# Kernel tuning notes

Measured on AMD Instinct MI355X. Metric: run time of the kernel, lower is better.

## Reference

```python
import jax, jax.numpy as jnp
import numpy as np

B, C, S = 16, 8, 128
DT, DX, DY = 0.001, 1.0, 1.0
NUM_STEPS = 10
EPS = 1e-6


def _thomas(a, b, c, d):
    """Batched Thomas tridiagonal solve. a,b,c,d: [M,N] rows; solve along N."""
    aT, bT, cT, dT = a.T, b.T, c.T, d.T  # [N, M]
    zero = jnp.zeros_like(dT[0])

    def fwd(carry, inp):
        cs_p, ds_p = carry
        ai, bi, ci, di = inp
        denom = bi - ai * cs_p + EPS  # i=0: cs_p=0 -> denom = b0 + eps (matches torch)
        cs = ci / denom
        ds = (di - ai * ds_p) / denom
        return (cs, ds), (cs, ds)

    _, (c_star, d_star) = jax.lax.scan(fwd, (zero, zero), (aT, bT, cT, dT))

    def bwd(x_next, inp):
        ci, di = inp
        x = di - ci * x_next
        return x, x

    _, xs = jax.lax.scan(bwd, d_star[-1], (c_star[:-1], d_star[:-1]), reverse=True)
    x = jnp.concatenate([xs, d_star[-1:]], axis=0)  # [N, M]
    return x.T


def _diffuse_rows(u2d, coeff):
    """Implicit 1D diffusion along last axis. u2d, coeff: [M,N]."""
    a = -coeff
    c = -coeff
    b = 1.0 + 2.0 * coeff
    b = b.at[:, 0].set(1.0 + coeff[:, 0])
    b = b.at[:, -1].set(1.0 + coeff[:, -1])
    return _thomas(a, b, c, u2d)


def _forward(u, alpha_base, beta_base, alpha_time_coeff, beta_time_coeff, channel_mixing):
    Bb, Cc, H, W = u.shape
    half = DT / 2.0
    t = 0.0
    for _ in range(NUM_STEPS):
        # x half-step (coefficient alpha at time t)
        alpha = jnp.clip(alpha_base + alpha_time_coeff * t, EPS, 10.0)
        u = jnp.einsum('dc,bchw->bdhw', channel_mixing, u)
        uf = u.reshape(Bb * Cc, H, W)
        af = jnp.broadcast_to(alpha[None], (Bb, Cc, H, W)).reshape(Bb * Cc, H, W)
        uf = _diffuse_rows(uf.reshape(-1, W), af.reshape(-1, W) * half / DX**2).reshape(Bb * Cc, H, W)
        t += half
        # y full step (coefficient beta at time t+dt/2)
        beta = jnp.clip(beta_base + beta_time_coeff * t, EPS, 10.0)
        bf = jnp.broadcast_to(beta[None], (Bb, Cc, H, W)).reshape(Bb * Cc, H, W)
        ut = uf.transpose(0, 2, 1).reshape(-1, H)
        bt = bf.transpose(0, 2, 1).reshape(-1, H)
        ut = _diffuse_rows(ut, bt * DT / DY**2)
        uf = ut.reshape(Bb * Cc, W, H).transpose(0, 2, 1)
        t += half
        # x half-step (coefficient alpha at time t+dt)
        alpha = jnp.clip(alpha_base + alpha_time_coeff * t, EPS, 10.0)
        af = jnp.broadcast_to(alpha[None], (Bb, Cc, H, W)).reshape(Bb * Cc, H, W)
        uf = _diffuse_rows(uf.reshape(-1, W), af.reshape(-1, W) * half / DX**2).reshape(Bb * Cc, H, W)
        u = uf.reshape(Bb, Cc, H, W)
    return u


def setup_inputs() -> dict:
    key = jax.random.key(0)
    k_u, k_cm, k_atc, k_btc = jax.random.split(key, 4)
    u = jax.random.normal(k_u, (B, C, S, S), dtype=jnp.float32)
    alpha_base = jnp.ones((C, S, S), dtype=jnp.float32)
    beta_base = jnp.ones((C, S, S), dtype=jnp.float32)
    alpha_time_coeff = jax.random.normal(k_atc, (C, S, S), dtype=jnp.float32) * 0.01
    beta_time_coeff = jax.random.normal(k_btc, (C, S, S), dtype=jnp.float32) * 0.01
    channel_mixing = jnp.eye(C, dtype=jnp.float32) + jax.random.normal(k_cm, (C, C), dtype=jnp.float32) * 0.01
    return {
        'u': u,
        'alpha_base': alpha_base,
        'beta_base': beta_base,
        'alpha_time_coeff': alpha_time_coeff,
        'beta_time_coeff': beta_time_coeff,
        'channel_mixing': channel_mixing,
    }


def reference(u, alpha_base, beta_base, alpha_time_coeff, beta_time_coeff, channel_mixing):
    return _forward(u, alpha_base, beta_base, alpha_time_coeff, beta_time_coeff, channel_mixing)
```

## Files before the change

### kernel.cpp

```cpp
#include <hip/hip_runtime.h>
#include <hip/hip_fp16.h>


constexpr int S_  = 128;
constexpr int RS  = 129;
constexpr float EPSF = 1e-6f;
constexpr int CSS = 8 * 128 * 128;

constexpr int SOFF_A = 0;
constexpr int SOFF_B = 64 * 128;
constexpr int SOFF_C = 128 * 128;
constexpr int SPOOL  = 192 * 128;

__device__ __forceinline__ int swad(int r, int b) {
    return r * 128 + (((b) ^ (r & 31)) << 2);
}

template <int N>
__device__ __forceinline__ void jrunN(const float (&e)[N], const float (&g)[N],
                                      float (&o)[N - 4]) {
    float x1[N];
    #pragma unroll
    for (int i = 1; i <= N - 2; ++i) x1[i] = fmaf(g[i], e[i - 1] + e[i + 1], e[i]);
    #pragma unroll
    for (int i = 2; i <= N - 3; ++i) o[i - 2] = fmaf(g[i], x1[i - 1] + x1[i + 1], e[i]);
}

__global__ __launch_bounds__(256) void coef_kernel(
    const float* __restrict__ ab, const float* __restrict__ atc,
    const float* __restrict__ bb, const float* __restrict__ btc,
    __half2* __restrict__ cf)
{
    for (int gc = blockIdx.x * 256 + threadIdx.x; gc < CSS; gc += gridDim.x * 256) {
        const int w = gc & 127, h = (gc >> 7) & 127;
        const float abv = ab[gc], atv = atc[gc], bbv = bb[gc], btv = btc[gc];
        const float nbY = (h == 0 || h == S_ - 1) ? 1.f : 2.f;
        const float nbX = (w == 0 || w == S_ - 1) ? 1.f : 2.f;
        for (int k = 0; k < 10; ++k) {
            const float ty = (2 * k + 1) * 0.0005f;
            const float tx = (2 * k + 2) * 0.0005f;
            float be = fminf(fmaxf(fmaf(btv, ty, bbv), EPSF), 10.f);
            float co = be * 0.001f;
            float rb = __builtin_amdgcn_rcpf(fmaf(nbY, co, 1.f) + EPSF);
            cf[k * CSS + gc] = __floats2half2_rn(rb * co, rb - 1.f);
            float al = fminf(fmaxf(fmaf(atv, tx, abv), EPSF), 10.f);
            co = al * 0.0005f;
            rb = __builtin_amdgcn_rcpf(fmaf(nbX, co, 1.f) + EPSF);
            cf[(10 + k) * CSS + gc] = __floats2half2_rn(rb * co, rb - 1.f);
        }
        float al = fminf(fmaxf(abv, EPSF), 10.f);
        float co = al * 0.0005f;
        float rb = __builtin_amdgcn_rcpf(fmaf(nbX, co, 1.f) + EPSF);
        cf[20 * CSS + gc] = __floats2half2_rn(rb * co, rb - 1.f);
    }
}

__global__ __launch_bounds__(512, 2) void head_kernel(
    const float* __restrict__ u0, __half* __restrict__ ud,
    const __half2* __restrict__ cfy, const __half2* __restrict__ cfx,
    const __half2* __restrict__ cfx0, const float* __restrict__ cm)
{
    constexpr int POOL   = 288 * RS;
    constexpr int OFF_A  = 0;
    constexpr int OFF_B  = 64 * RS;
    constexpr int OFF_CP = 192 * RS;
    constexpr int OFF_X0 = 96 * RS;
    __shared__ float sP[POOL];
    const int tid = threadIdx.x;
    const int b   = blockIdx.x >> 4;
    const int h0  = (blockIdx.x & 15) << 3;

    #pragma unroll
    for (int m = 0; m < 2; ++m) {
        const int col = tid + 512 * m;
        const int c = col >> 7, w = col & 127;
        #pragma unroll
        for (int hh = 0; hh < 12; ++hh) {
            const int gh = h0 - 2 + hh;
            float v = 0.f;
            if (gh >= 0 && gh < S_) v = u0[((b * 8 + c) * S_ + gh) * S_ + w];
            sP[(c * 12 + hh) * RS + w] = v;
        }
    }
    #pragma unroll
    for (int m = 0; m < 12; ++m) {
        const int task = tid + 512 * m;
        const int r = task >> 6, col2 = task & 63;
        const int c = r / 12, hh = r % 12;
        int gh = h0 - 2 + hh; gh = gh < 0 ? 0 : (gh >= S_ ? S_ - 1 : gh);
        const uint2 v = ((const uint2*)cfx0)[(c * S_ + gh) * 64 + col2];
        sP[OFF_CP + r * RS + col2 * 2]     = __uint_as_float(v.x);
        sP[OFF_CP + r * RS + col2 * 2 + 1] = __uint_as_float(v.y);
    }
    __syncthreads();
    {
        float M[64];
        #pragma unroll
        for (int i = 0; i < 64; ++i) M[i] = cm[i];
        #pragma unroll
        for (int m = 0; m < 3; ++m) {
            const int p = tid + 512 * m;
            const int hh = p >> 7, w = p & 127;
            float v[8], o[8];
            #pragma unroll
            for (int c = 0; c < 8; ++c) v[c] = sP[(c * 12 + hh) * RS + w];
            #pragma unroll
            for (int dd = 0; dd < 8; ++dd) {
                float a = 0.f;
                #pragma unroll
                for (int c = 0; c < 8; ++c) a = fmaf(M[dd * 8 + c], v[c], a);
                o[dd] = a;
            }
            #pragma unroll
            for (int c = 0; c < 8; ++c) sP[(c * 12 + hh) * RS + w] = o[c];
        }
    }
    __syncthreads();
    #pragma unroll
    for (int m = 0; m < 3; ++m) {
        const int task = tid + 512 * m;
        const int r96 = task % 96, wr = task / 96;
        const int hh = r96 % 12;
        const int gh = h0 - 2 + hh;
        const bool rowin = (gh >= 0 && gh < S_);
        const int w0 = wr * 8;
        float e[12], g[12];
        #pragma unroll
        for (int j = 0; j < 12; ++j) {
            const int wj = w0 - 2 + j;
            const bool win = (wj >= 0 && wj < S_);
            const float dv = win ? sP[r96 * RS + wj] : 0.f;
            uint cb = (rowin && win) ? __float_as_uint(sP[OFF_CP + r96 * RS + wj]) : 0u;
            const float2 f = __half22float2(*reinterpret_cast<__half2*>(&cb));
            e[j] = (1.f + f.y) * dv;
            g[j] = f.x;
        }
        float o[8]; jrunN<12>(e, g, o);
        #pragma unroll
        for (int i = 0; i < 8; ++i) sP[OFF_X0 + r96 * RS + w0 + i] = o[i];
    }
    __syncthreads();

    #pragma unroll
    for (int m = 0; m < 2; ++m) {
        const int col = tid + 512 * m;
        const int c = col >> 7, w = col & 127;
        float e[12], g[12];
        #pragma unroll
        for (int hh = 0; hh < 12; ++hh) {
            const int gh = h0 - 2 + hh;
            const bool inr = (gh >= 0 && gh < S_);
            const int ghc = inr ? gh : 0;
            const float dv = sP[OFF_X0 + (c * 12 + hh) * RS + w];
            const float2 f = __half22float2(cfy[(c * S_ + ghc) * S_ + w]);
            e[hh] = (1.f + f.y) * dv;
            g[hh] = inr ? f.x : 0.f;
        }
        float o[8]; jrunN<12>(e, g, o);
        #pragma unroll
        for (int i = 0; i < 8; ++i) sP[OFF_A + (c * 8 + i) * RS + w] = o[i];
    }
    __syncthreads();
    #pragma unroll
    for (int m = 0; m < 8; ++m) {
        const int task = tid + 512 * m;
        const int r = task >> 6, col2 = task & 63;
        const int c = r >> 3, ho = r & 7;
        const uint2 v = ((const uint2*)cfx)[(c * S_ + h0 + ho) * 64 + col2];
        sP[OFF_CP + r * RS + col2 * 2]     = __uint_as_float(v.x);
        sP[OFF_CP + r * RS + col2 * 2 + 1] = __uint_as_float(v.y);
    }
    __syncthreads();

    float rbk[2][12], gk[2][12], xo[2][8];
    #pragma unroll
    for (int m = 0; m < 2; ++m) {
        const int run = tid + 512 * m;
        const int r = run & 63, wr = run >> 6;
        const int w0 = wr * 8;
        float e[12];
        #pragma unroll
        for (int j = 0; j < 12; ++j) {
            const int wj = w0 - 2 + j;
            const bool win = (wj >= 0 && wj < S_);
            const float dv = win ? sP[OFF_A + r * RS + wj] : 0.f;
            uint cb = win ? __float_as_uint(sP[OFF_CP + r * RS + wj]) : 0u;
            const float2 f = __half22float2(*reinterpret_cast<__half2*>(&cb));
            rbk[m][j] = 1.f + f.y; gk[m][j] = f.x;
            e[j] = rbk[m][j] * dv;
        }
        jrunN<12>(e, gk[m], xo[m]);
    }
    #pragma unroll
    for (int m = 0; m < 2; ++m) {
        const int run = tid + 512 * m;
        const int r = run & 63, w0 = (run >> 6) * 8;
        #pragma unroll
        for (int i = 0; i < 8; ++i) sP[OFF_B + r * RS + w0 + i] = xo[m][i];
    }
    __syncthreads();
    {
        float M[64];
        #pragma unroll
        for (int i = 0; i < 64; ++i) M[i] = cm[i];
        #pragma unroll
        for (int m = 0; m < 2; ++m) {
            const int p = tid + 512 * m;
            const int ho = p >> 7, w = p & 127;
            float v[8], o[8];
            #pragma unroll
            for (int c = 0; c < 8; ++c) v[c] = sP[OFF_B + (c * 8 + ho) * RS + w];
            #pragma unroll
            for (int dd = 0; dd < 8; ++dd) {
                float a = 0.f;
                #pragma unroll
                for (int c = 0; c < 8; ++c) a = fmaf(M[dd * 8 + c], v[c], a);
                o[dd] = a;
            }
            #pragma unroll
            for (int c = 0; c < 8; ++c) sP[OFF_A + (c * 8 + ho) * RS + w] = o[c];
        }
    }
    __syncthreads();
    #pragma unroll
    for (int m = 0; m < 2; ++m) {
        const int run = tid + 512 * m;
        const int r = run & 63, wr = run >> 6;
        const int w0 = wr * 8;
        const int c = r >> 3, ho = r & 7;
        float e[12];
        #pragma unroll
        for (int j = 0; j < 12; ++j) {
            const int wj = w0 - 2 + j;
            const bool win = (wj >= 0 && wj < S_);
            const float dv = win ? sP[OFF_A + r * RS + wj] : 0.f;
            e[j] = rbk[m][j] * dv;
        }
        float o[8]; jrunN<12>(e, gk[m], o);
        __half2* d2 = (__half2*)&ud[((b * 8 + c) * S_ + h0 + ho) * S_ + w0];
        d2[0] = __floats2half2_rn(o[0], o[1]);
        d2[1] = __floats2half2_rn(o[2], o[3]);
        d2[2] = __floats2half2_rn(o[4], o[5]);
        d2[3] = __floats2half2_rn(o[6], o[7]);
    }
}

template <bool LASTK>
__global__ __launch_bounds__(512) void stepS_kernel(
    const __half* __restrict__ us, void* __restrict__ udst_,
    const __half2* __restrict__ cfy, const __half2* __restrict__ cfx,
    const float* __restrict__ cm)
{
    __shared__ __align__(16) float sP[SPOOL];
    const int tid = threadIdx.x;
    const int b   = blockIdx.x >> 4;
    const int h0  = (blockIdx.x & 15) << 3;

    {
        const int c  = tid >> 6;
        const int wp = tid & 63;
        const int wbase = 2 * wp;
        uint du[12]; uint2 dc[12];
        #pragma unroll
        for (int hh = 0; hh < 12; ++hh) {
            const int gh = h0 - 2 + hh;
            const bool inr = (gh >= 0 && gh < S_);
            const int ghc = inr ? gh : 0;
            du[hh] = inr ? *(const uint*)&us[((b * 8 + c) * S_ + ghc) * S_ + wbase] : 0u;
            dc[hh] = *(const uint2*)&cfy[(c * S_ + ghc) * S_ + wbase];
        }
        float o2[2][8];
        #pragma unroll
        for (int s = 0; s < 2; ++s) {
            float e[12], g[12];
            #pragma unroll
            for (int hh = 0; hh < 12; ++hh) {
                const int gh = h0 - 2 + hh;
                const bool inr = (gh >= 0 && gh < S_);
                uint ub = du[hh];
                __half2 hu = *reinterpret_cast<__half2*>(&ub);
                const float dv = s ? __high2float(hu) : __low2float(hu);
                uint cb = s ? dc[hh].y : dc[hh].x;
                const float2 f = __half22float2(*reinterpret_cast<__half2*>(&cb));
                e[hh] = (1.f + f.y) * dv;
                g[hh] = inr ? f.x : 0.f;
            }
            jrunN<12>(e, g, o2[s]);
        }
        #pragma unroll
        for (int i = 0; i < 8; ++i) {
            const int r = c * 8 + i;
            float2* p = (float2*)&sP[SOFF_A + r * 128 +
                                     (((wp >> 1) ^ (r & 31)) << 2) + 2 * (wp & 1)];
            *p = make_float2(o2[0][i], o2[1][i]);
        }
    }
    {
        const uint* cfxu = (const uint*)cfx;
        #pragma unroll
        for (int m = 0; m < 4; ++m) {
            const int task = tid + 512 * m;
            const int r = task >> 5, col4 = task & 31;
            const int c = r >> 3, ho = r & 7;
            const uint4 v = *(const uint4*)&cfxu[(c * S_ + h0 + ho) * S_ + col4 * 4];
            *(float4*)&sP[SOFF_C + swad(r, col4)] =
                make_float4(__uint_as_float(v.x), __uint_as_float(v.y),
                            __uint_as_float(v.z), __uint_as_float(v.w));
        }
    }
    __syncthreads();

    float rbk[2][12], gk[2][12], xo[2][8];
    #pragma unroll
    for (int m = 0; m < 2; ++m) {
        const int r  = tid & 63;
        const int wr = (tid >> 6) + 8 * m;
        const int w0 = wr * 8;
        float f[16]; uint cb[16];
        #pragma unroll
        for (int i = 0; i < 4; ++i) {
            const int bb = (w0 >> 2) - 1 + i;
            if (bb >= 0 && bb < 32) {
                const float4 va = *(const float4*)&sP[SOFF_A + swad(r, bb)];
                const float4 vc = *(const float4*)&sP[SOFF_C + swad(r, bb)];
                f[4 * i + 0] = va.x; f[4 * i + 1] = va.y;
                f[4 * i + 2] = va.z; f[4 * i + 3] = va.w;
                cb[4 * i + 0] = __float_as_uint(vc.x);
                cb[4 * i + 1] = __float_as_uint(vc.y);
                cb[4 * i + 2] = __float_as_uint(vc.z);
                cb[4 * i + 3] = __float_as_uint(vc.w);
            } else {
                f[4 * i + 0] = f[4 * i + 1] = f[4 * i + 2] = f[4 * i + 3] = 0.f;
                cb[4 * i + 0] = cb[4 * i + 1] = cb[4 * i + 2] = cb[4 * i + 3] = 0u;
            }
        }
        float e[12];
        #pragma unroll
        for (int j = 0; j < 12; ++j) {
            uint c_ = cb[j + 2];
            const float2 fc = __half22float2(*reinterpret_cast<__half2*>(&c_));
            rbk[m][j] = 1.f + fc.y; gk[m][j] = fc.x;
            e[j] = rbk[m][j] * f[j + 2];
        }
        jrunN<12>(e, gk[m], xo[m]);
    }

    if (LASTK) {
        float* ud = (float*)udst_;
        #pragma unroll
        for (int m = 0; m < 2; ++m) {
            const int r  = tid & 63;
            const int wr = (tid >> 6) + 8 * m;
            const int c = r >> 3, ho = r & 7;
            float4* dst4 = (float4*)&ud[((b * 8 + c) * S_ + h0 + ho) * S_ + wr * 8];
            dst4[0] = make_float4(xo[m][0], xo[m][1], xo[m][2], xo[m][3]);
            dst4[1] = make_float4(xo[m][4], xo[m][5], xo[m][6], xo[m][7]);
        }
    } else {
        #pragma unroll
        for (int m = 0; m < 2; ++m) {
            const int r  = tid & 63;
            const int wr = (tid >> 6) + 8 * m;
            *(float4*)&sP[SOFF_B + swad(r, 2 * wr)] =
                make_float4(xo[m][0], xo[m][1], xo[m][2], xo[m][3]);
            *(float4*)&sP[SOFF_B + swad(r, 2 * wr + 1)] =
                make_float4(xo[m][4], xo[m][5], xo[m][6], xo[m][7]);
        }
        __syncthreads();
        {
            float M[64];
            #pragma unroll
            for (int i = 0; i < 64; ++i) M[i] = cm[i];
            #pragma unroll
            for (int m = 0; m < 2; ++m) {
                const int p = tid + 512 * m;
                const int ho = p >> 7, w = p & 127;
                float v[8], o[8];
                #pragma unroll
                for (int c = 0; c < 8; ++c) {
                    const int r = c * 8 + ho;
                    v[c] = sP[SOFF_B + r * 128 + (((w >> 2) ^ (r & 31)) << 2) + (w & 3)];
                }
                #pragma unroll
                for (int dd = 0; dd < 8; ++dd) {
                    float a = 0.f;
                    #pragma unroll
                    for (int c = 0; c < 8; ++c) a = fmaf(M[dd * 8 + c], v[c], a);
                    o[dd] = a;
                }
                #pragma unroll
                for (int c = 0; c < 8; ++c) {
                    const int r = c * 8 + ho;
                    sP[SOFF_A + r * 128 + (((w >> 2) ^ (r & 31)) << 2) + (w & 3)] = o[c];
                }
            }
        }
        __syncthreads();
        __half* ud = (__half*)udst_;
        #pragma unroll
        for (int m = 0; m < 2; ++m) {
            const int r  = tid & 63;
            const int wr = (tid >> 6) + 8 * m;
            const int w0 = wr * 8;
            const int c = r >> 3, ho = r & 7;
            float f[16];
            #pragma unroll
            for (int i = 0; i < 4; ++i) {
                const int bb = (w0 >> 2) - 1 + i;
                if (bb >= 0 && bb < 32) {
                    const float4 va = *(const float4*)&sP[SOFF_A + swad(r, bb)];
                    f[4 * i + 0] = va.x; f[4 * i + 1] = va.y;
                    f[4 * i + 2] = va.z; f[4 * i + 3] = va.w;
                } else {
                    f[4 * i + 0] = f[4 * i + 1] = f[4 * i + 2] = f[4 * i + 3] = 0.f;
                }
            }
            float e[12];
            #pragma unroll
            for (int j = 0; j < 12; ++j) e[j] = rbk[m][j] * f[j + 2];
            float o[8]; jrunN<12>(e, gk[m], o);
            __half2 q0 = __floats2half2_rn(o[0], o[1]);
            __half2 q1 = __floats2half2_rn(o[2], o[3]);
            __half2 q2 = __floats2half2_rn(o[4], o[5]);
            __half2 q3 = __floats2half2_rn(o[6], o[7]);
            uint4 pk;
            pk.x = *reinterpret_cast<uint*>(&q0);
            pk.y = *reinterpret_cast<uint*>(&q1);
            pk.z = *reinterpret_cast<uint*>(&q2);
            pk.w = *reinterpret_cast<uint*>(&q3);
            *(uint4*)&ud[((b * 8 + c) * S_ + h0 + ho) * S_ + w0] = pk;
        }
    }
}

extern "C" void kernel_launch(void* const* d_in, const int* in_sizes, int n_in,
                              void* d_out, int out_size, void* d_ws, size_t ws_size,
                              hipStream_t stream) {
    const float* u_in = (const float*)d_in[0];
    const float* ab   = (const float*)d_in[1];
    const float* bbta = (const float*)d_in[2];
    const float* atc  = (const float*)d_in[3];
    const float* btc  = (const float*)d_in[4];
    const float* cm   = (const float*)d_in[5];
    float* uo = (float*)d_out;
    __half*  h1 = (__half*)d_ws;
    __half*  h2 = (__half*)((char*)d_ws + (8u << 20));
    __half2* cf = (__half2*)((char*)d_ws + (16u << 20));

    coef_kernel<<<dim3(512), dim3(256), 0, stream>>>(ab, atc, bbta, btc, cf);

    const dim3 g(256), blk(512);
    head_kernel<<<g, blk, 0, stream>>>(u_in, h1, cf + 0 * CSS, cf + 10 * CSS,
                                       cf + 20 * CSS, cm);
    const __half* s = h1; __half* d = h2;
    for (int k = 1; k <= 8; ++k) {
        stepS_kernel<false><<<g, blk, 0, stream>>>(s, d, cf + k * CSS,
                                                   cf + (10 + k) * CSS, cm);
        const __half* ns = d;
        d = (d == h2) ? h1 : h2;
        s = ns;
    }
    stepS_kernel<true><<<g, blk, 0, stream>>>(s, uo, cf + 9 * CSS,
                                              cf + 19 * CSS, cm);
}
```

Baseline: 152.7 us.

## Fuse time steps in pairs per kernel and fold coefficient computation into head

Replaces the per-step kernel chain with a kernel that advances two ADI steps per launch, using a wider halo (16 rows) in the y direction so the two steps can run without touching global memory in between. The separate coefficient kernel is removed: the head kernel computes the coefficients for its own first steps inline and writes the tables for later steps. This cuts the launch count from 11 to 5 and halves the fp16 intermediate traffic to global memory, at the cost of redundant halo computation, more shared memory (288 rows) and more register pressure.

```diff
diff --git a/kernel.cpp b/kernel.cpp
--- a/kernel.cpp
+++ b/kernel.cpp
@@ -3,17 +3,20 @@
 
 
 constexpr int S_  = 128;
-constexpr int RS  = 129;
 constexpr float EPSF = 1e-6f;
 constexpr int CSS = 8 * 128 * 128;
 
-constexpr int SOFF_A = 0;
-constexpr int SOFF_B = 64 * 128;
-constexpr int SOFF_C = 128 * 128;
-constexpr int SPOOL  = 192 * 128;
-
-__device__ __forceinline__ int swad(int r, int b) {
-    return r * 128 + (((b) ^ (r & 31)) << 2);
+constexpr int P0    = 0;
+constexpr int Q0    = 96 * 128;
+constexpr int C0    = 192 * 128;
+constexpr int ST0   = 96 * 128;
+constexpr int SPOOL = 288 * 128;
+
+__device__ __forceinline__ int swad4(int r, int b4) {
+    return r * 128 + (((b4) ^ (r & 31)) << 2);
+}
+__device__ __forceinline__ int swadw(int r, int w) {
+    return r * 128 + ((((w) >> 2) ^ (r & 31)) << 2) + ((w) & 3);
 }
 
 template <int N>
@@ -26,229 +29,29 @@
     for (int i = 2; i <= N - 3; ++i) o[i - 2] = fmaf(g[i], x1[i - 1] + x1[i + 1], e[i]);
 }
 
-__global__ __launch_bounds__(256) void coef_kernel(
-    const float* __restrict__ ab, const float* __restrict__ atc,
-    const float* __restrict__ bb, const float* __restrict__ btc,
-    __half2* __restrict__ cf)
-{
-    for (int gc = blockIdx.x * 256 + threadIdx.x; gc < CSS; gc += gridDim.x * 256) {
-        const int w = gc & 127, h = (gc >> 7) & 127;
-        const float abv = ab[gc], atv = atc[gc], bbv = bb[gc], btv = btc[gc];
-        const float nbY = (h == 0 || h == S_ - 1) ? 1.f : 2.f;
-        const float nbX = (w == 0 || w == S_ - 1) ? 1.f : 2.f;
-        for (int k = 0; k < 10; ++k) {
-            const float ty = (2 * k + 1) * 0.0005f;
-            const float tx = (2 * k + 2) * 0.0005f;
-            float be = fminf(fmaxf(fmaf(btv, ty, bbv), EPSF), 10.f);
-            float co = be * 0.001f;
-            float rb = __builtin_amdgcn_rcpf(fmaf(nbY, co, 1.f) + EPSF);
-            cf[k * CSS + gc] = __floats2half2_rn(rb * co, rb - 1.f);
-            float al = fminf(fmaxf(fmaf(atv, tx, abv), EPSF), 10.f);
-            co = al * 0.0005f;
-            rb = __builtin_amdgcn_rcpf(fmaf(nbX, co, 1.f) + EPSF);
-            cf[(10 + k) * CSS + gc] = __floats2half2_rn(rb * co, rb - 1.f);
-        }
-        float al = fminf(fmaxf(abv, EPSF), 10.f);
-        float co = al * 0.0005f;
-        float rb = __builtin_amdgcn_rcpf(fmaf(nbX, co, 1.f) + EPSF);
-        cf[20 * CSS + gc] = __floats2half2_rn(rb * co, rb - 1.f);
-    }
-}
-
-__global__ __launch_bounds__(512, 2) void head_kernel(
-    const float* __restrict__ u0, __half* __restrict__ ud,
-    const __half2* __restrict__ cfy, const __half2* __restrict__ cfx,
-    const __half2* __restrict__ cfx0, const float* __restrict__ cm)
-{
-    constexpr int POOL   = 288 * RS;
-    constexpr int OFF_A  = 0;
-    constexpr int OFF_B  = 64 * RS;
-    constexpr int OFF_CP = 192 * RS;
-    constexpr int OFF_X0 = 96 * RS;
-    __shared__ float sP[POOL];
-    const int tid = threadIdx.x;
-    const int b   = blockIdx.x >> 4;
-    const int h0  = (blockIdx.x & 15) << 3;
-
-    #pragma unroll
-    for (int m = 0; m < 2; ++m) {
-        const int col = tid + 512 * m;
-        const int c = col >> 7, w = col & 127;
-        #pragma unroll
-        for (int hh = 0; hh < 12; ++hh) {
-            const int gh = h0 - 2 + hh;
-            float v = 0.f;
-            if (gh >= 0 && gh < S_) v = u0[((b * 8 + c) * S_ + gh) * S_ + w];
-            sP[(c * 12 + hh) * RS + w] = v;
-        }
-    }
-    #pragma unroll
-    for (int m = 0; m < 12; ++m) {
-        const int task = tid + 512 * m;
-        const int r = task >> 6, col2 = task & 63;
-        const int c = r / 12, hh = r % 12;
-        int gh = h0 - 2 + hh; gh = gh < 0 ? 0 : (gh >= S_ ? S_ - 1 : gh);
-        const uint2 v = ((const uint2*)cfx0)[(c * S_ + gh) * 64 + col2];
-        sP[OFF_CP + r * RS + col2 * 2]     = __uint_as_float(v.x);
-        sP[OFF_CP + r * RS + col2 * 2 + 1] = __uint_as_float(v.y);
-    }
-    __syncthreads();
-    {
-        float M[64];
-        #pragma unroll
-        for (int i = 0; i < 64; ++i) M[i] = cm[i];
-        #pragma unroll
-        for (int m = 0; m < 3; ++m) {
-            const int p = tid + 512 * m;
-            const int hh = p >> 7, w = p & 127;
-            float v[8], o[8];
-            #pragma unroll
-            for (int c = 0; c < 8; ++c) v[c] = sP[(c * 12 + hh) * RS + w];
-            #pragma unroll
-            for (int dd = 0; dd < 8; ++dd) {
-                float a = 0.f;
-                #pragma unroll
-                for (int c = 0; c < 8; ++c) a = fmaf(M[dd * 8 + c], v[c], a);
-                o[dd] = a;
-            }
-            #pragma unroll
-            for (int c = 0; c < 8; ++c) sP[(c * 12 + hh) * RS + w] = o[c];
-        }
-    }
-    __syncthreads();
-    #pragma unroll
-    for (int m = 0; m < 3; ++m) {
-        const int task = tid + 512 * m;
-        const int r96 = task % 96, wr = task / 96;
-        const int hh = r96 % 12;
-        const int gh = h0 - 2 + hh;
-        const bool rowin = (gh >= 0 && gh < S_);
-        const int w0 = wr * 8;
-        float e[12], g[12];
-        #pragma unroll
-        for (int j = 0; j < 12; ++j) {
-            const int wj = w0 - 2 + j;
-            const bool win = (wj >= 0 && wj < S_);
-            const float dv = win ? sP[r96 * RS + wj] : 0.f;
-            uint cb = (rowin && win) ? __float_as_uint(sP[OFF_CP + r96 * RS + wj]) : 0u;
-            const float2 f = __half22float2(*reinterpret_cast<__half2*>(&cb));
-            e[j] = (1.f + f.y) * dv;
-            g[j] = f.x;
-        }
-        float o[8]; jrunN<12>(e, g, o);
-        #pragma unroll
-        for (int i = 0; i < 8; ++i) sP[OFF_X0 + r96 * RS + w0 + i] = o[i];
-    }
-    __syncthreads();
-
-    #pragma unroll
-    for (int m = 0; m < 2; ++m) {
-        const int col = tid + 512 * m;
-        const int c = col >> 7, w = col & 127;
-        float e[12], g[12];
-        #pragma unroll
-        for (int hh = 0; hh < 12; ++hh) {
-            const int gh = h0 - 2 + hh;
-            const bool inr = (gh >= 0 && gh < S_);
-            const int ghc = inr ? gh : 0;
-            const float dv = sP[OFF_X0 + (c * 12 + hh) * RS + w];
-            const float2 f = __half22float2(cfy[(c * S_ + ghc) * S_ + w]);
-            e[hh] = (1.f + f.y) * dv;
-            g[hh] = inr ? f.x : 0.f;
-        }
-        float o[8]; jrunN<12>(e, g, o);
-        #pragma unroll
-        for (int i = 0; i < 8; ++i) sP[OFF_A + (c * 8 + i) * RS + w] = o[i];
-    }
-    __syncthreads();
-    #pragma unroll
-    for (int m = 0; m < 8; ++m) {
-        const int task = tid + 512 * m;
-        const int r = task >> 6, col2 = task & 63;
-        const int c = r >> 3, ho = r & 7;
-        const uint2 v = ((const uint2*)cfx)[(c * S_ + h0 + ho) * 64 + col2];
-        sP[OFF_CP + r * RS + col2 * 2]     = __uint_as_float(v.x);
-        sP[OFF_CP + r * RS + col2 * 2 + 1] = __uint_as_float(v.y);
-    }
-    __syncthreads();
-
-    float rbk[2][12], gk[2][12], xo[2][8];
-    #pragma unroll
-    for (int m = 0; m < 2; ++m) {
-        const int run = tid + 512 * m;
-        const int r = run & 63, wr = run >> 6;
-        const int w0 = wr * 8;
-        float e[12];
-        #pragma unroll
-        for (int j = 0; j < 12; ++j) {
-            const int wj = w0 - 2 + j;
-            const bool win = (wj >= 0 && wj < S_);
-            const float dv = win ? sP[OFF_A + r * RS + wj] : 0.f;
-            uint cb = win ? __float_as_uint(sP[OFF_CP + r * RS + wj]) : 0u;
-            const float2 f = __half22float2(*reinterpret_cast<__half2*>(&cb));
-            rbk[m][j] = 1.f + f.y; gk[m][j] = f.x;
-            e[j] = rbk[m][j] * dv;
-        }
-        jrunN<12>(e, gk[m], xo[m]);
-    }
-    #pragma unroll
-    for (int m = 0; m < 2; ++m) {
-        const int run = tid + 512 * m;
-        const int r = run & 63, w0 = (run >> 6) * 8;
-        #pragma unroll
-        for (int i = 0; i < 8; ++i) sP[OFF_B + r * RS + w0 + i] = xo[m][i];
-    }
-    __syncthreads();
-    {
-        float M[64];
-        #pragma unroll
-        for (int i = 0; i < 64; ++i) M[i] = cm[i];
-        #pragma unroll
-        for (int m = 0; m < 2; ++m) {
-            const int p = tid + 512 * m;
-            const int ho = p >> 7, w = p & 127;
-            float v[8], o[8];
-            #pragma unroll
-            for (int c = 0; c < 8; ++c) v[c] = sP[OFF_B + (c * 8 + ho) * RS + w];
-            #pragma unroll
-            for (int dd = 0; dd < 8; ++dd) {
-                float a = 0.f;
-                #pragma unroll
-                for (int c = 0; c < 8; ++c) a = fmaf(M[dd * 8 + c], v[c], a);
-                o[dd] = a;
-            }
-            #pragma unroll
-            for (int c = 0; c < 8; ++c) sP[OFF_A + (c * 8 + ho) * RS + w] = o[c];
-        }
-    }
-    __syncthreads();
-    #pragma unroll
-    for (int m = 0; m < 2; ++m) {
-        const int run = tid + 512 * m;
-        const int r = run & 63, wr = run >> 6;
-        const int w0 = wr * 8;
-        const int c = r >> 3, ho = r & 7;
-        float e[12];
-        #pragma unroll
-        for (int j = 0; j < 12; ++j) {
-            const int wj = w0 - 2 + j;
-            const bool win = (wj >= 0 && wj < S_);
-            const float dv = win ? sP[OFF_A + r * RS + wj] : 0.f;
-            e[j] = rbk[m][j] * dv;
-        }
-        float o[8]; jrunN<12>(e, gk[m], o);
-        __half2* d2 = (__half2*)&ud[((b * 8 + c) * S_ + h0 + ho) * S_ + w0];
-        d2[0] = __floats2half2_rn(o[0], o[1]);
-        d2[1] = __floats2half2_rn(o[2], o[3]);
-        d2[2] = __floats2half2_rn(o[4], o[5]);
-        d2[3] = __floats2half2_rn(o[6], o[7]);
-    }
-}
-
-template <bool LASTK>
-__global__ __launch_bounds__(512) void stepS_kernel(
+#define TAPS_GATHER(REG_A, f, cb)                                              \
+    {                                                                          \
+        _Pragma("unroll")                                                      \
+        for (int i_ = 0; i_ < 4; ++i_) {                                       \
+            const int bb_ = 2 * wr - 1 + i_;                                   \
+            if (bb_ >= 0 && bb_ < 32) {                                        \
+                const float4 va_ = *(const float4*)&sP[(REG_A) + swad4(r, bb_)];\
+                const float4 vc_ = *(const float4*)&sP[C0 + swad4(r, bb_)];    \
+                f[4*i_+0]=va_.x; f[4*i_+1]=va_.y; f[4*i_+2]=va_.z; f[4*i_+3]=va_.w; \
+                cb[4*i_+0]=__float_as_uint(vc_.x); cb[4*i_+1]=__float_as_uint(vc_.y); \
+                cb[4*i_+2]=__float_as_uint(vc_.z); cb[4*i_+3]=__float_as_uint(vc_.w); \
+            } else {                                                           \
+                f[4*i_+0]=f[4*i_+1]=f[4*i_+2]=f[4*i_+3]=0.f;                   \
+                cb[4*i_+0]=cb[4*i_+1]=cb[4*i_+2]=cb[4*i_+3]=0u;                \
+            }                                                                  \
+        }                                                                      \
+    }
+
+template <bool LAST>
+__global__ __launch_bounds__(512) void pairS_kernel(
     const __half* __restrict__ us, void* __restrict__ udst_,
-    const __half2* __restrict__ cfy, const __half2* __restrict__ cfx,
+    const __half2* __restrict__ cfyA, const __half2* __restrict__ cfxA,
+    const __half2* __restrict__ cfyB, const __half2* __restrict__ cfxB,
     const float* __restrict__ cm)
 {
     __shared__ __align__(16) float sP[SPOOL];
@@ -257,25 +60,23 @@
     const int h0  = (blockIdx.x & 15) << 3;
 
     {
-        const int c  = tid >> 6;
-        const int wp = tid & 63;
-        const int wbase = 2 * wp;
-        uint du[12]; uint2 dc[12];
-        #pragma unroll
-        for (int hh = 0; hh < 12; ++hh) {
-            const int gh = h0 - 2 + hh;
+        const int c = tid >> 6, wp = tid & 63, wb = 2 * wp;
+        uint du[16]; uint2 dc[16];
+        #pragma unroll
+        for (int hh = 0; hh < 16; ++hh) {
+            const int gh = h0 - 4 + hh;
             const bool inr = (gh >= 0 && gh < S_);
             const int ghc = inr ? gh : 0;
-            du[hh] = inr ? *(const uint*)&us[((b * 8 + c) * S_ + ghc) * S_ + wbase] : 0u;
-            dc[hh] = *(const uint2*)&cfy[(c * S_ + ghc) * S_ + wbase];
-        }
-        float o2[2][8];
+            du[hh] = inr ? *(const uint*)&us[((b * 8 + c) * S_ + ghc) * S_ + wb] : 0u;
+            dc[hh] = *(const uint2*)&cfyA[(c * S_ + ghc) * S_ + wb];
+        }
+        float o2[2][12];
         #pragma unroll
         for (int s = 0; s < 2; ++s) {
-            float e[12], g[12];
-            #pragma unroll
-            for (int hh = 0; hh < 12; ++hh) {
-                const int gh = h0 - 2 + hh;
+            float e[16], g[16];
+            #pragma unroll
+            for (int hh = 0; hh < 16; ++hh) {
+                const int gh = h0 - 4 + hh;
                 const bool inr = (gh >= 0 && gh < S_);
                 uint ub = du[hh];
                 __half2 hu = *reinterpret_cast<__half2*>(&ub);
@@ -285,27 +86,140 @@
                 e[hh] = (1.f + f.y) * dv;
                 g[hh] = inr ? f.x : 0.f;
             }
+            jrunN<16>(e, g, o2[s]);
+        }
+        #pragma unroll
+        for (int i = 0; i < 12; ++i) {
+            const int r = c * 12 + i;
+            *(float2*)&sP[P0 + r * 128 + (((wp >> 1) ^ (r & 31)) << 2) + 2 * (wp & 1)]
+                = make_float2(o2[0][i], o2[1][i]);
+        }
+    }
+    {
+        const uint* cx = (const uint*)cfxA;
+        #pragma unroll
+        for (int m = 0; m < 6; ++m) {
+            const int task = tid + 512 * m;
+            const int r = task >> 5, b4 = task & 31;
+            const int c = r / 12, ha = r - c * 12;
+            int gh = h0 - 2 + ha; gh = gh < 0 ? 0 : (gh >= S_ ? S_ - 1 : gh);
+            const uint4 v = *(const uint4*)&cx[(c * S_ + gh) * S_ + b4 * 4];
+            *(float4*)&sP[C0 + swad4(r, b4)] = make_float4(
+                __uint_as_float(v.x), __uint_as_float(v.y),
+                __uint_as_float(v.z), __uint_as_float(v.w));
+        }
+    }
+    __syncthreads();
+
+    #pragma unroll
+    for (int m = 0; m < 3; ++m) {
+        const int r  = (tid & 31) + 32 * m;
+        const int wr = tid >> 5;
+        float f[16]; uint cb[16];
+        TAPS_GATHER(P0, f, cb)
+        float e[12], g[12];
+        #pragma unroll
+        for (int j = 0; j < 12; ++j) {
+            uint c_ = cb[j + 2];
+            const float2 fc = __half22float2(*reinterpret_cast<__half2*>(&c_));
+            e[j] = (1.f + fc.y) * f[j + 2];
+            g[j] = fc.x;
+        }
+        float o[8]; jrunN<12>(e, g, o);
+        *(float4*)&sP[Q0 + swad4(r, 2 * wr)]     = make_float4(o[0], o[1], o[2], o[3]);
+        *(float4*)&sP[Q0 + swad4(r, 2 * wr + 1)] = make_float4(o[4], o[5], o[6], o[7]);
+    }
+    __syncthreads();
+    {
+        float M[64];
+        #pragma unroll
+        for (int i = 0; i < 64; ++i) M[i] = cm[i];
+        #pragma unroll
+        for (int m = 0; m < 3; ++m) {
+            const int p = tid + 512 * m;
+            const int ha = p >> 7, w = p & 127;
+            float v[8], o[8];
+            #pragma unroll
+            for (int c = 0; c < 8; ++c) v[c] = sP[Q0 + swadw(c * 12 + ha, w)];
+            #pragma unroll
+            for (int dd = 0; dd < 8; ++dd) {
+                float a = 0.f;
+                #pragma unroll
+                for (int c = 0; c < 8; ++c) a = fmaf(M[dd * 8 + c], v[c], a);
+                o[dd] = a;
+            }
+            #pragma unroll
+            for (int c = 0; c < 8; ++c) sP[Q0 + swadw(c * 12 + ha, w)] = o[c];
+        }
+    }
+    __syncthreads();
+    #pragma unroll
+    for (int m = 0; m < 3; ++m) {
+        const int r  = (tid & 31) + 32 * m;
+        const int wr = tid >> 5;
+        float f[16]; uint cb[16];
+        TAPS_GATHER(Q0, f, cb)
+        float e[12], g[12];
+        #pragma unroll
+        for (int j = 0; j < 12; ++j) {
+            uint c_ = cb[j + 2];
+            const float2 fc = __half22float2(*reinterpret_cast<__half2*>(&c_));
+            e[j] = (1.f + fc.y) * f[j + 2];
+            g[j] = fc.x;
+        }
+        float o[8]; jrunN<12>(e, g, o);
+        *(float4*)&sP[P0 + swad4(r, 2 * wr)]     = make_float4(o[0], o[1], o[2], o[3]);
+        *(float4*)&sP[P0 + swad4(r, 2 * wr + 1)] = make_float4(o[4], o[5], o[6], o[7]);
+    }
+    __syncthreads();
+
+    {
+        const int c = tid >> 6, wp = tid & 63, wb = 2 * wp;
+        float2 dp[12]; uint2 dc[12];
+        #pragma unroll
+        for (int hh = 0; hh < 12; ++hh) {
+            const int gh = h0 - 2 + hh;
+            const bool inr = (gh >= 0 && gh < S_);
+            const int ghc = inr ? gh : 0;
+            const int r = c * 12 + hh;
+            dp[hh] = *(const float2*)&sP[P0 + r * 128 +
+                                         (((wp >> 1) ^ (r & 31)) << 2) + 2 * (wp & 1)];
+            dc[hh] = *(const uint2*)&cfyB[(c * S_ + ghc) * S_ + wb];
+        }
+        float o2[2][8];
+        #pragma unroll
+        for (int s = 0; s < 2; ++s) {
+            float e[12], g[12];
+            #pragma unroll
+            for (int hh = 0; hh < 12; ++hh) {
+                const int gh = h0 - 2 + hh;
+                const bool inr = (gh >= 0 && gh < S_);
+                const float dv = s ? dp[hh].y : dp[hh].x;
+                uint cb = s ? dc[hh].y : dc[hh].x;
+                const float2 f = __half22float2(*reinterpret_cast<__half2*>(&cb));
+                e[hh] = (1.f + f.y) * dv;
+                g[hh] = inr ? f.x : 0.f;
+            }
             jrunN<12>(e, g, o2[s]);
         }
         #pragma unroll
         for (int i = 0; i < 8; ++i) {
             const int r = c * 8 + i;
-            float2* p = (float2*)&sP[SOFF_A + r * 128 +
-                                     (((wp >> 1) ^ (r & 31)) << 2) + 2 * (wp & 1)];
-            *p = make_float2(o2[0][i], o2[1][i]);
-        }
-    }
-    {
-        const uint* cfxu = (const uint*)cfx;
+            *(float2*)&sP[Q0 + r * 128 + (((wp >> 1) ^ (r & 31)) << 2) + 2 * (wp & 1)]
+                = make_float2(o2[0][i], o2[1][i]);
+        }
+    }
+    {
+        const uint* cx = (const uint*)cfxB;
         #pragma unroll
         for (int m = 0; m < 4; ++m) {
             const int task = tid + 512 * m;
-            const int r = task >> 5, col4 = task & 31;
+            const int r = task >> 5, b4 = task & 31;
             const int c = r >> 3, ho = r & 7;
-            const uint4 v = *(const uint4*)&cfxu[(c * S_ + h0 + ho) * S_ + col4 * 4];
-            *(float4*)&sP[SOFF_C + swad(r, col4)] =
-                make_float4(__uint_as_float(v.x), __uint_as_float(v.y),
-                            __uint_as_float(v.z), __uint_as_float(v.w));
+            const uint4 v = *(const uint4*)&cx[(c * S_ + h0 + ho) * S_ + b4 * 4];
+            *(float4*)&sP[C0 + swad4(r, b4)] = make_float4(
+                __uint_as_float(v.x), __uint_as_float(v.y),
+                __uint_as_float(v.z), __uint_as_float(v.w));
         }
     }
     __syncthreads();
@@ -315,25 +229,8 @@
     for (int m = 0; m < 2; ++m) {
         const int r  = tid & 63;
         const int wr = (tid >> 6) + 8 * m;
-        const int w0 = wr * 8;
         float f[16]; uint cb[16];
-        #pragma unroll
-        for (int i = 0; i < 4; ++i) {
-            const int bb = (w0 >> 2) - 1 + i;
-            if (bb >= 0 && bb < 32) {
-                const float4 va = *(const float4*)&sP[SOFF_A + swad(r, bb)];
-                const float4 vc = *(const float4*)&sP[SOFF_C + swad(r, bb)];
-                f[4 * i + 0] = va.x; f[4 * i + 1] = va.y;
-                f[4 * i + 2] = va.z; f[4 * i + 3] = va.w;
-                cb[4 * i + 0] = __float_as_uint(vc.x);
-                cb[4 * i + 1] = __float_as_uint(vc.y);
-                cb[4 * i + 2] = __float_as_uint(vc.z);
-                cb[4 * i + 3] = __float_as_uint(vc.w);
-            } else {
-                f[4 * i + 0] = f[4 * i + 1] = f[4 * i + 2] = f[4 * i + 3] = 0.f;
-                cb[4 * i + 0] = cb[4 * i + 1] = cb[4 * i + 2] = cb[4 * i + 3] = 0u;
-            }
-        }
+        TAPS_GATHER(Q0, f, cb)
         float e[12];
         #pragma unroll
         for (int j = 0; j < 12; ++j) {
@@ -345,7 +242,7 @@
         jrunN<12>(e, gk[m], xo[m]);
     }
 
-    if (LASTK) {
+    if (LAST) {
         float* ud = (float*)udst_;
         #pragma unroll
         for (int m = 0; m < 2; ++m) {
@@ -361,10 +258,8 @@
         for (int m = 0; m < 2; ++m) {
             const int r  = tid & 63;
             const int wr = (tid >> 6) + 8 * m;
-            *(float4*)&sP[SOFF_B + swad(r, 2 * wr)] =
-                make_float4(xo[m][0], xo[m][1], xo[m][2], xo[m][3]);
-            *(float4*)&sP[SOFF_B + swad(r, 2 * wr + 1)] =
-                make_float4(xo[m][4], xo[m][5], xo[m][6], xo[m][7]);
+            *(float4*)&sP[P0 + swad4(r, 2 * wr)]     = make_float4(xo[m][0], xo[m][1], xo[m][2], xo[m][3]);
+            *(float4*)&sP[P0 + swad4(r, 2 * wr + 1)] = make_float4(xo[m][4], xo[m][5], xo[m][6], xo[m][7]);
         }
         __syncthreads();
         {
@@ -377,10 +272,7 @@
                 const int ho = p >> 7, w = p & 127;
                 float v[8], o[8];
                 #pragma unroll
-                for (int c = 0; c < 8; ++c) {
-                    const int r = c * 8 + ho;
-                    v[c] = sP[SOFF_B + r * 128 + (((w >> 2) ^ (r & 31)) << 2) + (w & 3)];
-                }
+                for (int c = 0; c < 8; ++c) v[c] = sP[P0 + swadw(c * 8 + ho, w)];
                 #pragma unroll
                 for (int dd = 0; dd < 8; ++dd) {
                     float a = 0.f;
@@ -389,10 +281,7 @@
                     o[dd] = a;
                 }
                 #pragma unroll
-                for (int c = 0; c < 8; ++c) {
-                    const int r = c * 8 + ho;
-                    sP[SOFF_A + r * 128 + (((w >> 2) ^ (r & 31)) << 2) + (w & 3)] = o[c];
-                }
+                for (int c = 0; c < 8; ++c) sP[P0 + swadw(c * 8 + ho, w)] = o[c];
             }
         }
         __syncthreads();
@@ -401,18 +290,16 @@
         for (int m = 0; m < 2; ++m) {
             const int r  = tid & 63;
             const int wr = (tid >> 6) + 8 * m;
-            const int w0 = wr * 8;
             const int c = r >> 3, ho = r & 7;
             float f[16];
             #pragma unroll
             for (int i = 0; i < 4; ++i) {
-                const int bb = (w0 >> 2) - 1 + i;
+                const int bb = 2 * wr - 1 + i;
                 if (bb >= 0 && bb < 32) {
-                    const float4 va = *(const float4*)&sP[SOFF_A + swad(r, bb)];
-                    f[4 * i + 0] = va.x; f[4 * i + 1] = va.y;
-                    f[4 * i + 2] = va.z; f[4 * i + 3] = va.w;
+                    const float4 va = *(const float4*)&sP[P0 + swad4(r, bb)];
+                    f[4*i+0]=va.x; f[4*i+1]=va.y; f[4*i+2]=va.z; f[4*i+3]=va.w;
                 } else {
-                    f[4 * i + 0] = f[4 * i + 1] = f[4 * i + 2] = f[4 * i + 3] = 0.f;
+                    f[4*i+0]=f[4*i+1]=f[4*i+2]=f[4*i+3]=0.f;
                 }
             }
             float e[12];
@@ -428,7 +315,380 @@
             pk.y = *reinterpret_cast<uint*>(&q1);
             pk.z = *reinterpret_cast<uint*>(&q2);
             pk.w = *reinterpret_cast<uint*>(&q3);
-            *(uint4*)&ud[((b * 8 + c) * S_ + h0 + ho) * S_ + w0] = pk;
+            *(uint4*)&ud[((b * 8 + c) * S_ + h0 + ho) * S_ + wr * 8] = pk;
+        }
+    }
+}
+
+__global__ __launch_bounds__(512) void head2_kernel(
+    const float* __restrict__ u0, __half* __restrict__ ud,
+    const float* __restrict__ ab, const float* __restrict__ atc,
+    const float* __restrict__ bb, const float* __restrict__ btc,
+    const float* __restrict__ cm, __half2* __restrict__ cf)
+{
+    __shared__ __align__(16) float sP[SPOOL];
+    const int tid = threadIdx.x;
+    const int b   = blockIdx.x >> 4;
+    const int h0  = (blockIdx.x & 15) << 3;
+    const float dt2 = 0.0005f;
+
+    #pragma unroll
+    for (int m = 0; m < 8; ++m) {
+        const int task = tid + 512 * m;
+        const int r = task >> 5, b4 = task & 31;
+        const int c = r >> 4, hh = r & 15;
+        const int gh = h0 - 4 + hh;
+        float4 v = make_float4(0.f, 0.f, 0.f, 0.f);
+        if (gh >= 0 && gh < S_) v = *(const float4*)&u0[((b * 8 + c) * S_ + gh) * S_ + 4 * b4];
+        *(float4*)&sP[ST0 + swad4(r, b4)] = v;
+    }
+    __syncthreads();
+    {
+        float M[64];
+        #pragma unroll
+        for (int i = 0; i < 64; ++i) M[i] = cm[i];
+        #pragma unroll
+        for (int m = 0; m < 4; ++m) {
+            const int p = tid + 512 * m;
+            const int hh = p >> 7, w = p & 127;
+            float v[8], o[8];
+            #pragma unroll
+            for (int c = 0; c < 8; ++c) v[c] = sP[ST0 + swadw(c * 16 + hh, w)];
+            #pragma unroll
+            for (int dd = 0; dd < 8; ++dd) {
+                float a = 0.f;
+                #pragma unroll
+                for (int c = 0; c < 8; ++c) a = fmaf(M[dd * 8 + c], v[c], a);
+                o[dd] = a;
+            }
+            #pragma unroll
+            for (int c = 0; c < 8; ++c) sP[ST0 + swadw(c * 16 + hh, w)] = o[c];
+        }
+    }
+    __syncthreads();
+    {
+        float xh[4][8];
+        #pragma unroll
+        for (int m = 0; m < 4; ++m) {
+            const int r  = (tid & 31) + 32 * m;
+            const int wr = tid >> 5;
+            const int w0 = wr * 8;
+            const int c = r >> 4, hh = r & 15;
+            const int gh = h0 - 4 + hh;
+            const bool rowin = (gh >= 0 && gh < S_);
+            float f[16];
+            #pragma unroll
+            for (int i = 0; i < 4; ++i) {
+                const int bb4 = 2 * wr - 1 + i;
+                if (bb4 >= 0 && bb4 < 32) {
+                    const float4 va = *(const float4*)&sP[ST0 + swad4(r, bb4)];
+                    f[4*i+0]=va.x; f[4*i+1]=va.y; f[4*i+2]=va.z; f[4*i+3]=va.w;
+                } else {
+                    f[4*i+0]=f[4*i+1]=f[4*i+2]=f[4*i+3]=0.f;
+                }
+            }
+            float e[12], g[12];
+            #pragma unroll
+            for (int j = 0; j < 12; ++j) {
+                const int wj = w0 - 2 + j;
+                const bool win = (wj >= 0 && wj < S_);
+                float co = 0.f;
+                if (rowin && win) {
+                    float al = ab[(c * S_ + gh) * S_ + wj];
+                    co = fminf(fmaxf(al, EPSF), 10.f) * 0.0005f;
+                }
+                const float nb = (wj == 0 || wj == S_ - 1) ? 1.f : 2.f;
+                const float rb = __builtin_amdgcn_rcpf(fmaf(nb, co, 1.f) + EPSF);
+                e[j] = rb * f[j + 2]; g[j] = rb * co;
+            }
+            jrunN<12>(e, g, xh[m]);
+        }
+        __syncthreads();
+        #pragma unroll
+        for (int m = 0; m < 4; ++m) {
+            const int r  = (tid & 31) + 32 * m;
+            const int wr = tid >> 5;
+            *(float4*)&sP[ST0 + swad4(r, 2 * wr)]     = make_float4(xh[m][0], xh[m][1], xh[m][2], xh[m][3]);
+            *(float4*)&sP[ST0 + swad4(r, 2 * wr + 1)] = make_float4(xh[m][4], xh[m][5], xh[m][6], xh[m][7]);
+        }
+    }
+    __syncthreads();
+    {
+        const int c = tid >> 6, wp = tid & 63, wb = 2 * wp;
+        float o2[2][12];
+        #pragma unroll
+        for (int s = 0; s < 2; ++s) {
+            float e[16], g[16];
+            #pragma unroll
+            for (int hh = 0; hh < 16; ++hh) {
+                const int gh = h0 - 4 + hh;
+                const bool inr = (gh >= 0 && gh < S_);
+                const int ghc = inr ? gh : 0;
+                const int r = c * 16 + hh;
+                const float2 d2 = *(const float2*)&sP[ST0 + r * 128 +
+                                    (((wp >> 1) ^ (r & 31)) << 2) + 2 * (wp & 1)];
+                const float dv = s ? d2.y : d2.x;
+                const float2 b2 = *(const float2*)&bb[(c * S_ + ghc) * S_ + wb];
+                const float2 t2 = *(const float2*)&btc[(c * S_ + ghc) * S_ + wb];
+                float be = fmaf(s ? t2.y : t2.x, 1 * dt2, s ? b2.y : b2.x);
+                be = fminf(fmaxf(be, EPSF), 10.f);
+                const float co = inr ? be * 0.001f : 0.f;
+                const float nb = (gh == 0 || gh == S_ - 1) ? 1.f : 2.f;
+                const float rb = __builtin_amdgcn_rcpf(fmaf(nb, co, 1.f) + EPSF);
+                e[hh] = rb * dv; g[hh] = rb * co;
+            }
+            jrunN<16>(e, g, o2[s]);
+        }
+        #pragma unroll
+        for (int i = 0; i < 12; ++i) {
+            const int r = c * 12 + i;
+            *(float2*)&sP[P0 + r * 128 + (((wp >> 1) ^ (r & 31)) << 2) + 2 * (wp & 1)]
+                = make_float2(o2[0][i], o2[1][i]);
+        }
+    }
+    __syncthreads();
+    #pragma unroll
+    for (int m = 0; m < 6; ++m) {
+        const int task = tid + 512 * m;
+        const int r = task >> 5, b4 = task & 31;
+        const int c = r / 12, ha = r - c * 12;
+        int gh = h0 - 2 + ha; gh = gh < 0 ? 0 : (gh >= S_ ? S_ - 1 : gh);
+        const float4 a4 = *(const float4*)&ab[(c * S_ + gh) * S_ + 4 * b4];
+        const float4 t4 = *(const float4*)&atc[(c * S_ + gh) * S_ + 4 * b4];
+        uint pk[4];
+        #pragma unroll
+        for (int l = 0; l < 4; ++l) {
+            const int w = 4 * b4 + l;
+            const float av = l == 0 ? a4.x : (l == 1 ? a4.y : (l == 2 ? a4.z : a4.w));
+            const float tv = l == 0 ? t4.x : (l == 1 ? t4.y : (l == 2 ? t4.z : t4.w));
+            float al = fminf(fmaxf(fmaf(tv, 2 * dt2, av), EPSF), 10.f);
+            const float co = al * 0.0005f;
+            const float nb = (w == 0 || w == S_ - 1) ? 1.f : 2.f;
+            const float rb = __builtin_amdgcn_rcpf(fmaf(nb, co, 1.f) + EPSF);
+            __half2 hp = __floats2half2_rn(rb * co, rb - 1.f);
+            pk[l] = *reinterpret_cast<uint*>(&hp);
+        }
+        *(float4*)&sP[C0 + swad4(r, b4)] = make_float4(
+            __uint_as_float(pk[0]), __uint_as_float(pk[1]),
+            __uint_as_float(pk[2]), __uint_as_float(pk[3]));
+    }
+    __syncthreads();
+    #pragma unroll
+    for (int m = 0; m < 3; ++m) {
+        const int r  = (tid & 31) + 32 * m;
+        const int wr = tid >> 5;
+        float f[16]; uint cb[16];
+        TAPS_GATHER(P0, f, cb)
+        float e[12], g[12];
+        #pragma unroll
+        for (int j = 0; j < 12; ++j) {
+            uint c_ = cb[j + 2];
+            const float2 fc = __half22float2(*reinterpret_cast<__half2*>(&c_));
+            e[j] = (1.f + fc.y) * f[j + 2];
+            g[j] = fc.x;
+        }
+        float o[8]; jrunN<12>(e, g, o);
+        *(float4*)&sP[Q0 + swad4(r, 2 * wr)]     = make_float4(o[0], o[1], o[2], o[3]);
+        *(float4*)&sP[Q0 + swad4(r, 2 * wr + 1)] = make_float4(o[4], o[5], o[6], o[7]);
+    }
+    __syncthreads();
+    {
+        float M[64];
+        #pragma unroll
+        for (int i = 0; i < 64; ++i) M[i] = cm[i];
+        #pragma unroll
+        for (int m = 0; m < 3; ++m) {
+            const int p = tid + 512 * m;
+            const int ha = p >> 7, w = p & 127;
+            float v[8], o[8];
+            #pragma unroll
+            for (int c = 0; c < 8; ++c) v[c] = sP[Q0 + swadw(c * 12 + ha, w)];
+            #pragma unroll
+            for (int dd = 0; dd < 8; ++dd) {
+                float a = 0.f;
+                #pragma unroll
+                for (int c = 0; c < 8; ++c) a = fmaf(M[dd * 8 + c], v[c], a);
+                o[dd] = a;
+            }
+            #pragma unroll
+            for (int c = 0; c < 8; ++c) sP[Q0 + swadw(c * 12 + ha, w)] = o[c];
+        }
+    }
+    __syncthreads();
+    #pragma unroll
+    for (int m = 0; m < 3; ++m) {
+        const int r  = (tid & 31) + 32 * m;
+        const int wr = tid >> 5;
+        float f[16]; uint cb[16];
+        TAPS_GATHER(Q0, f, cb)
+        float e[12], g[12];
+        #pragma unroll
+        for (int j = 0; j < 12; ++j) {
+            uint c_ = cb[j + 2];
+            const float2 fc = __half22float2(*reinterpret_cast<__half2*>(&c_));
+            e[j] = (1.f + fc.y) * f[j + 2];
+            g[j] = fc.x;
+        }
+        float o[8]; jrunN<12>(e, g, o);
+        *(float4*)&sP[P0 + swad4(r, 2 * wr)]     = make_float4(o[0], o[1], o[2], o[3]);
+        *(float4*)&sP[P0 + swad4(r, 2 * wr + 1)] = make_float4(o[4], o[5], o[6], o[7]);
+    }
+    __syncthreads();
+    {
+        const int c = tid >> 6, wp = tid & 63, wb = 2 * wp;
+        float o2[2][8];
+        #pragma unroll
+        for (int s = 0; s < 2; ++s) {
+            float e[12], g[12];
+            #pragma unroll
+            for (int hh = 0; hh < 12; ++hh) {
+                const int gh = h0 - 2 + hh;
+                const bool inr = (gh >= 0 && gh < S_);
+                const int ghc = inr ? gh : 0;
+                const int r = c * 12 + hh;
+                const float2 d2 = *(const float2*)&sP[P0 + r * 128 +
+                                    (((wp >> 1) ^ (r & 31)) << 2) + 2 * (wp & 1)];
+                const float dv = s ? d2.y : d2.x;
+                const float2 b2 = *(const float2*)&bb[(c * S_ + ghc) * S_ + wb];
+                const float2 t2 = *(const float2*)&btc[(c * S_ + ghc) * S_ + wb];
+                float be = fmaf(s ? t2.y : t2.x, 3 * dt2, s ? b2.y : b2.x);
+                be = fminf(fmaxf(be, EPSF), 10.f);
+                const float co = inr ? be * 0.001f : 0.f;
+                const float nb = (gh == 0 || gh == S_ - 1) ? 1.f : 2.f;
+                const float rb = __builtin_amdgcn_rcpf(fmaf(nb, co, 1.f) + EPSF);
+                e[hh] = rb * dv; g[hh] = rb * co;
+            }
+            jrunN<12>(e, g, o2[s]);
+        }
+        #pragma unroll
+        for (int i = 0; i < 8; ++i) {
+            const int r = c * 8 + i;
+            *(float2*)&sP[Q0 + r * 128 + (((wp >> 1) ^ (r & 31)) << 2) + 2 * (wp & 1)]
+                = make_float2(o2[0][i], o2[1][i]);
+        }
+    }
+    #pragma unroll
+    for (int m = 0; m < 4; ++m) {
+        const int task = tid + 512 * m;
+        const int r = task >> 5, b4 = task & 31;
+        const int c = r >> 3, ho = r & 7;
+        const int gh = h0 + ho;
+        const float4 a4 = *(const float4*)&ab[(c * S_ + gh) * S_ + 4 * b4];
+        const float4 t4 = *(const float4*)&atc[(c * S_ + gh) * S_ + 4 * b4];
+        uint pk[4];
+        #pragma unroll
+        for (int l = 0; l < 4; ++l) {
+            const int w = 4 * b4 + l;
+            const float av = l == 0 ? a4.x : (l == 1 ? a4.y : (l == 2 ? a4.z : a4.w));
+            const float tv = l == 0 ? t4.x : (l == 1 ? t4.y : (l == 2 ? t4.z : t4.w));
+            float al = fminf(fmaxf(fmaf(tv, 4 * dt2, av), EPSF), 10.f);
+            const float co = al * 0.0005f;
+            const float nb = (w == 0 || w == S_ - 1) ? 1.f : 2.f;
+            const float rb = __builtin_amdgcn_rcpf(fmaf(nb, co, 1.f) + EPSF);
+            __half2 hp = __floats2half2_rn(rb * co, rb - 1.f);
+            pk[l] = *reinterpret_cast<uint*>(&hp);
+        }
+        *(float4*)&sP[C0 + swad4(r, b4)] = make_float4(
+            __uint_as_float(pk[0]), __uint_as_float(pk[1]),
+            __uint_as_float(pk[2]), __uint_as_float(pk[3]));
+    }
+    __syncthreads();
+    float rbk[2][12], gk[2][12], xo[2][8];
+    #pragma unroll
+    for (int m = 0; m < 2; ++m) {
+        const int r  = tid & 63;
+        const int wr = (tid >> 6) + 8 * m;
+        float f[16]; uint cb[16];
+        TAPS_GATHER(Q0, f, cb)
+        float e[12];
+        #pragma unroll
+        for (int j = 0; j < 12; ++j) {
+            uint c_ = cb[j + 2];
+            const float2 fc = __half22float2(*reinterpret_cast<__half2*>(&c_));
+            rbk[m][j] = 1.f + fc.y; gk[m][j] = fc.x;
+            e[j] = rbk[m][j] * f[j + 2];
+        }
+        jrunN<12>(e, gk[m], xo[m]);
+    }
+    #pragma unroll
+    for (int m = 0; m < 2; ++m) {
+        const int r  = tid & 63;
+        const int wr = (tid >> 6) + 8 * m;
+        *(float4*)&sP[P0 + swad4(r, 2 * wr)]     = make_float4(xo[m][0], xo[m][1], xo[m][2], xo[m][3]);
+        *(float4*)&sP[P0 + swad4(r, 2 * wr + 1)] = make_float4(xo[m][4], xo[m][5], xo[m][6], xo[m][7]);
+    }
+    __syncthreads();
+    {
+        float M[64];
+        #pragma unroll
+        for (int i = 0; i < 64; ++i) M[i] = cm[i];
+        #pragma unroll
+        for (int m = 0; m < 2; ++m) {
+            const int p = tid + 512 * m;
+            const int ho = p >> 7, w = p & 127;
+            float v[8], o[8];
+            #pragma unroll
+            for (int c = 0; c < 8; ++c) v[c] = sP[P0 + swadw(c * 8 + ho, w)];
+            #pragma unroll
+            for (int dd = 0; dd < 8; ++dd) {
+                float a = 0.f;
+                #pragma unroll
+                for (int c = 0; c < 8; ++c) a = fmaf(M[dd * 8 + c], v[c], a);
+                o[dd] = a;
+            }
+            #pragma unroll
+            for (int c = 0; c < 8; ++c) sP[P0 + swadw(c * 8 + ho, w)] = o[c];
+        }
+    }
+    __syncthreads();
+    #pragma unroll
+    for (int m = 0; m < 2; ++m) {
+        const int r  = tid & 63;
+        const int wr = (tid >> 6) + 8 * m;
+        const int c = r >> 3, ho = r & 7;
+        float f[16];
+        #pragma unroll
+        for (int i = 0; i < 4; ++i) {
+            const int bb4 = 2 * wr - 1 + i;
+            if (bb4 >= 0 && bb4 < 32) {
+                const float4 va = *(const float4*)&sP[P0 + swad4(r, bb4)];
+                f[4*i+0]=va.x; f[4*i+1]=va.y; f[4*i+2]=va.z; f[4*i+3]=va.w;
+            } else {
+                f[4*i+0]=f[4*i+1]=f[4*i+2]=f[4*i+3]=0.f;
+            }
+        }
+        float e[12];
+        #pragma unroll
+        for (int j = 0; j < 12; ++j) e[j] = rbk[m][j] * f[j + 2];
+        float o[8]; jrunN<12>(e, gk[m], o);
+        __half2 q0 = __floats2half2_rn(o[0], o[1]);
+        __half2 q1 = __floats2half2_rn(o[2], o[3]);
+        __half2 q2 = __floats2half2_rn(o[4], o[5]);
+        __half2 q3 = __floats2half2_rn(o[6], o[7]);
+        uint4 pk;
+        pk.x = *reinterpret_cast<uint*>(&q0);
+        pk.y = *reinterpret_cast<uint*>(&q1);
+        pk.z = *reinterpret_cast<uint*>(&q2);
+        pk.w = *reinterpret_cast<uint*>(&q3);
+        *(uint4*)&ud[((b * 8 + c) * S_ + h0 + ho) * S_ + wr * 8] = pk;
+    }
+
+    {
+        const int idx = blockIdx.x * 512 + tid;
+        const float abv = ab[idx], atv = atc[idx], bbv = bb[idx], btv = btc[idx];
+        const int w = idx & 127, h = (idx >> 7) & 127;
+        const float nbY = (h == 0 || h == S_ - 1) ? 1.f : 2.f;
+        const float nbX = (w == 0 || w == S_ - 1) ? 1.f : 2.f;
+        #pragma unroll
+        for (int k = 2; k < 10; ++k) {
+            float be = fminf(fmaxf(fmaf(btv, (2 * k + 1) * dt2, bbv), EPSF), 10.f);
+            float co = be * 0.001f;
+            float rb = __builtin_amdgcn_rcpf(fmaf(nbY, co, 1.f) + EPSF);
+            cf[k * CSS + idx] = __floats2half2_rn(rb * co, rb - 1.f);
+            float al = fminf(fmaxf(fmaf(atv, (2 * k + 2) * dt2, abv), EPSF), 10.f);
+            co = al * 0.0005f;
+            rb = __builtin_amdgcn_rcpf(fmaf(nbX, co, 1.f) + EPSF);
+            cf[(10 + k) * CSS + idx] = __floats2half2_rn(rb * co, rb - 1.f);
         }
     }
 }
@@ -447,19 +707,14 @@
     __half*  h2 = (__half*)((char*)d_ws + (8u << 20));
     __half2* cf = (__half2*)((char*)d_ws + (16u << 20));
 
-    coef_kernel<<<dim3(512), dim3(256), 0, stream>>>(ab, atc, bbta, btc, cf);
-
     const dim3 g(256), blk(512);
-    head_kernel<<<g, blk, 0, stream>>>(u_in, h1, cf + 0 * CSS, cf + 10 * CSS,
-                                       cf + 20 * CSS, cm);
-    const __half* s = h1; __half* d = h2;
-    for (int k = 1; k <= 8; ++k) {
-        stepS_kernel<false><<<g, blk, 0, stream>>>(s, d, cf + k * CSS,
-                                                   cf + (10 + k) * CSS, cm);
-        const __half* ns = d;
-        d = (d == h2) ? h1 : h2;
-        s = ns;
-    }
-    stepS_kernel<true><<<g, blk, 0, stream>>>(s, uo, cf + 9 * CSS,
-                                              cf + 19 * CSS, cm);
+    head2_kernel<<<g, blk, 0, stream>>>(u_in, h1, ab, atc, bbta, btc, cm, cf);
+    pairS_kernel<false><<<g, blk, 0, stream>>>(h1, h2, cf + 2 * CSS, cf + 12 * CSS,
+                                               cf + 3 * CSS, cf + 13 * CSS, cm);
+    pairS_kernel<false><<<g, blk, 0, stream>>>(h2, h1, cf + 4 * CSS, cf + 14 * CSS,
+                                               cf + 5 * CSS, cf + 15 * CSS, cm);
+    pairS_kernel<false><<<g, blk, 0, stream>>>(h1, h2, cf + 6 * CSS, cf + 16 * CSS,
+                                               cf + 7 * CSS, cf + 17 * CSS, cm);
+    pairS_kernel<true><<<g, blk, 0, stream>>>(h2, uo, cf + 8 * CSS, cf + 18 * CSS,
+                                              cf + 9 * CSS, cf + 19 * CSS, cm);
 }
```

Result: slower. 164.0 us (+7.4%).
